# Kernel optimization log

Measured on AMD Instinct MI355X. Metric: run time of the kernel, lower is better.

The kernel has to match this reference:

```python
import jax, jax.numpy as jnp
import numpy as np

N_NODES = 100000
N_EDGES = 640000
HIDDEN = 128


def setup_inputs() -> dict:
    key = jax.random.key(0)
    k_h, k_e, k_w1, k_b1, k_w2, k_b2 = jax.random.split(key, 6)
    h = jax.random.normal(k_h, (N_NODES, HIDDEN), dtype=jnp.float32)
    edge_index = jax.random.randint(k_e, (2, N_EDGES), 0, N_NODES, dtype=jnp.int64)
    # nn.Linear default init: U(-1/sqrt(fan_in), 1/sqrt(fan_in))
    lim1 = 1.0 / np.sqrt(2 * HIDDEN)
    W1 = jax.random.uniform(k_w1, (2 * HIDDEN, HIDDEN), jnp.float32, -lim1, lim1)
    b1 = jax.random.uniform(k_b1, (HIDDEN,), jnp.float32, -lim1, lim1)
    lim2 = 1.0 / np.sqrt(HIDDEN)
    W2 = jax.random.uniform(k_w2, (HIDDEN, 1), jnp.float32, -lim2, lim2)
    b2 = jax.random.uniform(k_b2, (1,), jnp.float32, -lim2, lim2)
    return {"h": h, "edge_index": edge_index, "W1": W1, "b1": b1, "W2": W2, "b2": b2}


def reference(h, edge_index, W1, b1, W2, b2):
    src, dst = edge_index[0], edge_index[1]
    # cat([h[src], h[dst]]) @ W1 == h[src] @ W1[:H] + h[dst] @ W1[H:]
    W1s, W1d = W1[:HIDDEN], W1[HIDDEN:]
    x = h[src] @ W1s + h[dst] @ W1d + b1          # [E, H]
    x = jax.nn.relu(x)
    score = x @ W2 + b2                            # [E, 1]
    return score.squeeze(-1)                       # [E]
```

## Files before the change

### kernel.cpp

```cpp
#include <hip/hip_runtime.h>

#define HIDDEN 128

typedef _Float16 f16x8 __attribute__((ext_vector_type(8)));
typedef _Float16 f16x4 __attribute__((ext_vector_type(4)));
typedef _Float16 f16x2 __attribute__((ext_vector_type(2)));
typedef __fp16   fp16v2 __attribute__((ext_vector_type(2)));
typedef float f32x4 __attribute__((ext_vector_type(4)));

__global__ __launch_bounds__(64) void prep_w(const float* __restrict__ W1,
                                             _Float16* __restrict__ Wpk) {
  const int blk = blockIdx.x;
  const int jt = blk >> 2;
  const int kt = blk & 3;
  const int lane = threadIdx.x;
  const int col = jt * 16 + (lane & 15);
  const int kbase = kt * 32 + (lane >> 4) * 8;
  f16x8 v;
#pragma unroll
  for (int j = 0; j < 8; ++j) {
    const int k = kbase + j;
    const float w = (col < HIDDEN) ? W1[k * HIDDEN + col]
                                   : W1[(HIDDEN + k) * HIDDEN + (col - HIDDEN)];
    v[j] = (_Float16)w;
  }
  *reinterpret_cast<f16x8*>(Wpk + ((size_t)blk * 64 + lane) * 8) = v;
}

__global__ __launch_bounds__(256) void gemm_mfma_v9(
    const float* __restrict__ h, const _Float16* __restrict__ Wpk,
    const float* __restrict__ b1, _Float16* __restrict__ Af,
    _Float16* __restrict__ Bf, int n_nodes, int ntiles) {
  __shared__ __align__(16) char out_lds[4 * 16 * 528];

  const int tid = threadIdx.x;
  const int lane = tid & 63;
  const int wave = tid >> 6;
  const int nl = lane & 15;
  const int kgrp = lane >> 4;
  const int jt0 = wave * 4;
  const int t0 = blockIdx.x * 4;
  if (t0 >= ntiles) return;

  const f16x8* wp = reinterpret_cast<const f16x8*>(Wpk);
  f16x8 wfrag[4][4];
#pragma unroll
  for (int j4 = 0; j4 < 4; ++j4)
#pragma unroll
    for (int kt = 0; kt < 4; ++kt)
      wfrag[j4][kt] = wp[((jt0 + j4) * 4 + kt) * 64 + lane];

  f32x4 binit[4];
#pragma unroll
  for (int j4 = 0; j4 < 4; ++j4) {
    const int jt = jt0 + j4;
    if (jt < 8) {
      binit[j4] = *reinterpret_cast<const f32x4*>(b1 + jt * 16 + kgrp * 4);
    } else {
      binit[j4][0] = 0.f; binit[j4][1] = 0.f; binit[j4][2] = 0.f; binit[j4][3] = 0.f;
    }
  }

  float4 buf0[8], buf1[8];
  f16x8 hfrag[4];

  auto LOAD = [&](float4* buf, int tile) {
    int node = tile * 16 + nl;
    if (node >= n_nodes) node = 0;
    const float4* hp = reinterpret_cast<const float4*>(h) +
                       (size_t)node * 32 + kgrp * 2;
#pragma unroll
    for (int kt = 0; kt < 4; ++kt) {
      buf[kt * 2]     = hp[kt * 8];
      buf[kt * 2 + 1] = hp[kt * 8 + 1];
    }
  };

  auto CVT = [&](const float4* buf) {
#pragma unroll
    for (int kt = 0; kt < 4; ++kt) {
      const float4 v0 = buf[kt * 2];
      const float4 v1 = buf[kt * 2 + 1];
      const fp16v2 p0 = __builtin_amdgcn_cvt_pkrtz(v0.x, v0.y);
      const fp16v2 p1 = __builtin_amdgcn_cvt_pkrtz(v0.z, v0.w);
      const fp16v2 p2 = __builtin_amdgcn_cvt_pkrtz(v1.x, v1.y);
      const fp16v2 p3 = __builtin_amdgcn_cvt_pkrtz(v1.z, v1.w);
      hfrag[kt][0] = (_Float16)p0[0]; hfrag[kt][1] = (_Float16)p0[1];
      hfrag[kt][2] = (_Float16)p1[0]; hfrag[kt][3] = (_Float16)p1[1];
      hfrag[kt][4] = (_Float16)p2[0]; hfrag[kt][5] = (_Float16)p2[1];
      hfrag[kt][6] = (_Float16)p3[0]; hfrag[kt][7] = (_Float16)p3[1];
    }
  };

  auto COMPUTE_DSWRITE = [&](int i) {
    f32x4 acc[4];
#pragma unroll
    for (int j4 = 0; j4 < 4; ++j4) acc[j4] = binit[j4];
#pragma unroll
    for (int kt = 0; kt < 4; ++kt)
#pragma unroll
      for (int j4 = 0; j4 < 4; ++j4)
        acc[j4] = __builtin_amdgcn_mfma_f32_16x16x32_f16(
            wfrag[j4][kt], hfrag[kt], acc[j4], 0, 0, 0);
#pragma unroll
    for (int j4 = 0; j4 < 4; ++j4) {
      const int jt = jt0 + j4;
      const int byte = i * 8448 + nl * 528 +
                       ((jt & 7) * 16 + kgrp * 4) * 2 + ((jt >= 8) ? 256 : 0);
      f16x4 v;
      v[0] = (_Float16)acc[j4][0];
      v[1] = (_Float16)acc[j4][1];
      v[2] = (_Float16)acc[j4][2];
      v[3] = (_Float16)acc[j4][3];
      *reinterpret_cast<f16x4*>(out_lds + byte) = v;
    }
  };

  LOAD(buf0, t0);
  LOAD(buf1, t0 + 1);
  CVT(buf0); LOAD(buf0, t0 + 2); COMPUTE_DSWRITE(0);
  CVT(buf1); LOAD(buf1, t0 + 3); COMPUTE_DSWRITE(1);
  CVT(buf0);                     COMPUTE_DSWRITE(2);
  CVT(buf1);                     COMPUTE_DSWRITE(3);

  __syncthreads();

  const int cn = tid >> 4;
  const int seg = tid & 15;
#pragma unroll
  for (int i = 0; i < 4; ++i) {
    const int node = (t0 + i) * 16 + cn;
    if (node < n_nodes) {
      const f16x8 a = *reinterpret_cast<const f16x8*>(
          out_lds + i * 8448 + cn * 528 + seg * 16);
      const f16x8 b = *reinterpret_cast<const f16x8*>(
          out_lds + i * 8448 + cn * 528 + 256 + seg * 16);
      *reinterpret_cast<f16x8*>(Af + (size_t)node * HIDDEN + seg * 8) = a;
      *reinterpret_cast<f16x8*>(Bf + (size_t)node * HIDDEN + seg * 8) = b;
    }
  }
}

__global__ __launch_bounds__(256) void edge_score_v5(
    const int* __restrict__ ei, const _Float16* __restrict__ Af,
    const _Float16* __restrict__ Bf, const float* __restrict__ W2,
    const float* __restrict__ b2, float* __restrict__ out, int n_edges) {
  const int wid = (int)((blockIdx.x * 256 + threadIdx.x) >> 6);
  const int lane = threadIdx.x & 63;
  const int e0 = wid * 16;
  if (e0 >= n_edges) return;

  int srcs[16], dsts[16];
  if (e0 + 16 <= n_edges) {
    const int4* sp = reinterpret_cast<const int4*>(ei + e0);
    const int4* dp = reinterpret_cast<const int4*>(ei + n_edges + e0);
#pragma unroll
    for (int q = 0; q < 4; ++q) {
      const int4 s4 = sp[q], d4 = dp[q];
      srcs[q * 4] = s4.x; srcs[q * 4 + 1] = s4.y; srcs[q * 4 + 2] = s4.z; srcs[q * 4 + 3] = s4.w;
      dsts[q * 4] = d4.x; dsts[q * 4 + 1] = d4.y; dsts[q * 4 + 2] = d4.z; dsts[q * 4 + 3] = d4.w;
    }
  } else {
#pragma unroll
    for (int k = 0; k < 16; ++k) {
      const int e = (e0 + k < n_edges) ? e0 + k : n_edges - 1;
      srcs[k] = ei[e];
      dsts[k] = ei[n_edges + e];
    }
  }

  const char* Afc = (const char*)Af;
  const char* Bfc = (const char*)Bf;
  const unsigned int loff = (unsigned int)(lane << 2);

  f16x2 av[16], bv[16];
#pragma unroll
  for (int k = 0; k < 16; ++k) {
    av[k] = *reinterpret_cast<const f16x2*>(Afc + (((unsigned int)srcs[k] << 8) + loff));
    bv[k] = *reinterpret_cast<const f16x2*>(Bfc + (((unsigned int)dsts[k] << 8) + loff));
  }
  __builtin_amdgcn_sched_barrier(0);

  const float2 w2v = reinterpret_cast<const float2*>(W2)[lane];
  const fp16v2 w2h = __builtin_amdgcn_cvt_pkrtz(w2v.x, w2v.y);
  const _Float16 h0 = (_Float16)0.f;

  float p[16];
#pragma unroll
  for (int k = 0; k < 16; ++k) {
    f16x2 s = av[k] + bv[k];
    s[0] = s[0] > h0 ? s[0] : h0;
    s[1] = s[1] > h0 ? s[1] : h0;
    p[k] = __builtin_amdgcn_fdot2(__builtin_bit_cast(fp16v2, s), w2h, 0.f, false);
  }

  auto mrg = [&](float a, float b, int off) {
    const float as = a + __shfl_xor(a, off, 64);
    const float bs = b + __shfl_xor(b, off, 64);
    return (lane & off) ? bs : as;
  };
  float q[8];
#pragma unroll
  for (int i = 0; i < 8; ++i) q[i] = mrg(p[2 * i], p[2 * i + 1], 1);
  float r[4];
#pragma unroll
  for (int i = 0; i < 4; ++i) r[i] = mrg(q[2 * i], q[2 * i + 1], 2);
  float s2[2];
#pragma unroll
  for (int i = 0; i < 2; ++i) s2[i] = mrg(r[2 * i], r[2 * i + 1], 4);
  float t = mrg(s2[0], s2[1], 8);
  t += __shfl_xor(t, 16, 64);
  t += __shfl_xor(t, 32, 64);

  if (lane < 16 && e0 + lane < n_edges) out[e0 + lane] = t + b2[0];
}

__global__ __launch_bounds__(256) void fused_fallback(
    const float* __restrict__ h, const int* __restrict__ ei,
    const float* __restrict__ W1, const float* __restrict__ b1,
    const float* __restrict__ W2, const float* __restrict__ b2,
    float* __restrict__ out, int n_edges) {
  const int e = (int)((blockIdx.x * 256 + threadIdx.x) >> 6);
  const int lane = threadIdx.x & 63;
  if (e >= n_edges) return;
  const int src = ei[e], dst = ei[n_edges + e];
  const float* hs = h + (size_t)src * HIDDEN;
  const float* hd = h + (size_t)dst * HIDDEN;
  float acc0 = b1[lane], acc1 = b1[lane + 64];
  for (int k = 0; k < HIDDEN; ++k) {
    const float s = hs[k], d = hd[k];
    acc0 = fmaf(s, W1[k * HIDDEN + lane], acc0);
    acc0 = fmaf(d, W1[(k + HIDDEN) * HIDDEN + lane], acc0);
    acc1 = fmaf(s, W1[k * HIDDEN + lane + 64], acc1);
    acc1 = fmaf(d, W1[(k + HIDDEN) * HIDDEN + lane + 64], acc1);
  }
  acc0 = acc0 > 0.f ? acc0 : 0.f;
  acc1 = acc1 > 0.f ? acc1 : 0.f;
  float p = fmaf(acc0, W2[lane], acc1 * W2[lane + 64]);
#pragma unroll
  for (int off = 32; off >= 1; off >>= 1) p += __shfl_down(p, off, 64);
  if (lane == 0) out[e] = p + b2[0];
}

extern "C" void kernel_launch(void* const* d_in, const int* in_sizes, int n_in,
                              void* d_out, int out_size, void* d_ws, size_t ws_size,
                              hipStream_t stream) {
  const float* h  = (const float*)d_in[0];
  const int*   ei = (const int*)d_in[1];
  const float* W1 = (const float*)d_in[2];
  const float* b1 = (const float*)d_in[3];
  const float* W2 = (const float*)d_in[4];
  const float* b2 = (const float*)d_in[5];
  float* out = (float*)d_out;

  const int n_nodes = in_sizes[0] / HIDDEN;
  const int n_edges = in_sizes[1] / 2;

  const size_t wpk_halfs  = 64 * 64 * 8;
  const size_t proj_halfs = (size_t)n_nodes * HIDDEN;
  const size_t need = (wpk_halfs + 2 * proj_halfs) * sizeof(_Float16);

  if (ws_size >= need) {
    _Float16* Wpk = (_Float16*)d_ws;
    _Float16* A   = Wpk + wpk_halfs;
    _Float16* B   = A + proj_halfs;

    prep_w<<<64, 64, 0, stream>>>(W1, Wpk);

    const int ntiles = (n_nodes + 15) / 16;
    const int gblocks = (ntiles + 3) / 4;
    gemm_mfma_v9<<<gblocks, 256, 0, stream>>>(h, Wpk, b1, A, B, n_nodes, ntiles);

    const int nwaves = (n_edges + 15) / 16;
    const int eblocks = (nwaves + 3) / 4;
    edge_score_v5<<<eblocks, 256, 0, stream>>>(ei, A, B, W2, b2, out, n_edges);
  } else {
    const int eblocks = (n_edges + 3) / 4;
    fused_fallback<<<eblocks, 256, 0, stream>>>(h, ei, W1, b1, W2, b2, out, n_edges);
  }
}
```

Baseline: 89.16 us.

## Stage node rows through swizzled LDS with coalesced loads in projection GEMM

The node-projection kernel now has each block handle 32 nodes. Threads load h with fully coalesced float4 reads, convert to fp16 and store into an XOR-swizzled LDS staging buffer, and the MFMA operands are then read from that buffer. Before, each lane loaded strided fragments from global memory directly, with register double-buffering over 4 tiles. The new layout is meant to improve global load coalescing and raise block count/occupancy, at the cost of an extra barrier and the loss of load/compute overlap within a block. A scheduling barrier in the edge kernel is also removed.

```diff
diff --git a/kernel.cpp b/kernel.cpp
--- a/kernel.cpp
+++ b/kernel.cpp
@@ -27,11 +27,12 @@
   *reinterpret_cast<f16x8*>(Wpk + ((size_t)blk * 64 + lane) * 8) = v;
 }
 
-__global__ __launch_bounds__(256) void gemm_mfma_v9(
+__global__ __launch_bounds__(256) void gemm_mfma_v10(
     const float* __restrict__ h, const _Float16* __restrict__ Wpk,
     const float* __restrict__ b1, _Float16* __restrict__ Af,
-    _Float16* __restrict__ Bf, int n_nodes, int ntiles) {
-  __shared__ __align__(16) char out_lds[4 * 16 * 528];
+    _Float16* __restrict__ Bf, int n_nodes) {
+  __shared__ __align__(16) char stage[32 * 256];
+  __shared__ __align__(16) char obuf[32 * 528];
 
   const int tid = threadIdx.x;
   const int lane = tid & 63;
@@ -39,8 +40,7 @@
   const int nl = lane & 15;
   const int kgrp = lane >> 4;
   const int jt0 = wave * 4;
-  const int t0 = blockIdx.x * 4;
-  if (t0 >= ntiles) return;
+  const int node0 = blockIdx.x * 32;
 
   const f16x8* wp = reinterpret_cast<const f16x8*>(Wpk);
   f16x8 wfrag[4][4];
@@ -61,80 +61,77 @@
     }
   }
 
-  float4 buf0[8], buf1[8];
-  f16x8 hfrag[4];
-
-  auto LOAD = [&](float4* buf, int tile) {
-    int node = tile * 16 + nl;
-    if (node >= n_nodes) node = 0;
-    const float4* hp = reinterpret_cast<const float4*>(h) +
-                       (size_t)node * 32 + kgrp * 2;
+  float4 sbuf[4];
+#pragma unroll
+  for (int q = 0; q < 4; ++q) {
+    const int lin = q * 2048 + tid * 8;
+    int node = node0 + (lin >> 8);
+    if (node >= n_nodes) node = n_nodes - 1;
+    sbuf[q] = *reinterpret_cast<const float4*>(
+        reinterpret_cast<const char*>(h) + (size_t)node * 512 + (lin & 255) * 2);
+  }
+#pragma unroll
+  for (int q = 0; q < 4; ++q) {
+    const int lin = q * 2048 + tid * 8;
+    const int row = lin >> 8;
+    const int col = lin & 255;
+    const fp16v2 p0 = __builtin_amdgcn_cvt_pkrtz(sbuf[q].x, sbuf[q].y);
+    const fp16v2 p1 = __builtin_amdgcn_cvt_pkrtz(sbuf[q].z, sbuf[q].w);
+    f16x4 v;
+    v[0] = (_Float16)p0[0]; v[1] = (_Float16)p0[1];
+    v[2] = (_Float16)p1[0]; v[3] = (_Float16)p1[1];
+    const int dst = row * 256 + (col ^ ((row & 7) << 4));
+    *reinterpret_cast<f16x4*>(stage + dst) = v;
+  }
+  __syncthreads();
+
+  f32x4 acc[2][4];
+#pragma unroll
+  for (int s = 0; s < 2; ++s)
+#pragma unroll
+    for (int j4 = 0; j4 < 4; ++j4) acc[s][j4] = binit[j4];
+
+#pragma unroll
+  for (int s = 0; s < 2; ++s) {
+    const int row = s * 16 + nl;
 #pragma unroll
     for (int kt = 0; kt < 4; ++kt) {
-      buf[kt * 2]     = hp[kt * 8];
-      buf[kt * 2 + 1] = hp[kt * 8 + 1];
-    }
-  };
-
-  auto CVT = [&](const float4* buf) {
-#pragma unroll
-    for (int kt = 0; kt < 4; ++kt) {
-      const float4 v0 = buf[kt * 2];
-      const float4 v1 = buf[kt * 2 + 1];
-      const fp16v2 p0 = __builtin_amdgcn_cvt_pkrtz(v0.x, v0.y);
-      const fp16v2 p1 = __builtin_amdgcn_cvt_pkrtz(v0.z, v0.w);
-      const fp16v2 p2 = __builtin_amdgcn_cvt_pkrtz(v1.x, v1.y);
-      const fp16v2 p3 = __builtin_amdgcn_cvt_pkrtz(v1.z, v1.w);
-      hfrag[kt][0] = (_Float16)p0[0]; hfrag[kt][1] = (_Float16)p0[1];
-      hfrag[kt][2] = (_Float16)p1[0]; hfrag[kt][3] = (_Float16)p1[1];
-      hfrag[kt][4] = (_Float16)p2[0]; hfrag[kt][5] = (_Float16)p2[1];
-      hfrag[kt][6] = (_Float16)p3[0]; hfrag[kt][7] = (_Float16)p3[1];
-    }
-  };
-
-  auto COMPUTE_DSWRITE = [&](int i) {
-    f32x4 acc[4];
-#pragma unroll
-    for (int j4 = 0; j4 < 4; ++j4) acc[j4] = binit[j4];
-#pragma unroll
-    for (int kt = 0; kt < 4; ++kt)
+      const int addr = row * 256 + ((kt * 64 + kgrp * 16) ^ ((row & 7) << 4));
+      const f16x8 hf = *reinterpret_cast<const f16x8*>(stage + addr);
 #pragma unroll
       for (int j4 = 0; j4 < 4; ++j4)
-        acc[j4] = __builtin_amdgcn_mfma_f32_16x16x32_f16(
-            wfrag[j4][kt], hfrag[kt], acc[j4], 0, 0, 0);
+        acc[s][j4] = __builtin_amdgcn_mfma_f32_16x16x32_f16(
+            wfrag[j4][kt], hf, acc[s][j4], 0, 0, 0);
+    }
+  }
+
+#pragma unroll
+  for (int s = 0; s < 2; ++s) {
+    const int row = s * 16 + nl;
 #pragma unroll
     for (int j4 = 0; j4 < 4; ++j4) {
       const int jt = jt0 + j4;
-      const int byte = i * 8448 + nl * 528 +
-                       ((jt & 7) * 16 + kgrp * 4) * 2 + ((jt >= 8) ? 256 : 0);
+      const int byte = row * 528 + ((jt & 7) * 16 + kgrp * 4) * 2 +
+                       ((jt >= 8) ? 256 : 0);
       f16x4 v;
-      v[0] = (_Float16)acc[j4][0];
-      v[1] = (_Float16)acc[j4][1];
-      v[2] = (_Float16)acc[j4][2];
-      v[3] = (_Float16)acc[j4][3];
-      *reinterpret_cast<f16x4*>(out_lds + byte) = v;
-    }
-  };
-
-  LOAD(buf0, t0);
-  LOAD(buf1, t0 + 1);
-  CVT(buf0); LOAD(buf0, t0 + 2); COMPUTE_DSWRITE(0);
-  CVT(buf1); LOAD(buf1, t0 + 3); COMPUTE_DSWRITE(1);
-  CVT(buf0);                     COMPUTE_DSWRITE(2);
-  CVT(buf1);                     COMPUTE_DSWRITE(3);
-
+      v[0] = (_Float16)acc[s][j4][0];
+      v[1] = (_Float16)acc[s][j4][1];
+      v[2] = (_Float16)acc[s][j4][2];
+      v[3] = (_Float16)acc[s][j4][3];
+      *reinterpret_cast<f16x4*>(obuf + byte) = v;
+    }
+  }
   __syncthreads();
 
-  const int cn = tid >> 4;
+  const int cs = tid >> 4;
   const int seg = tid & 15;
 #pragma unroll
-  for (int i = 0; i < 4; ++i) {
-    const int node = (t0 + i) * 16 + cn;
+  for (int half = 0; half < 2; ++half) {
+    const int cn = half * 16 + cs;
+    const int node = node0 + cn;
     if (node < n_nodes) {
-      const f16x8 a = *reinterpret_cast<const f16x8*>(
-          out_lds + i * 8448 + cn * 528 + seg * 16);
-      const f16x8 b = *reinterpret_cast<const f16x8*>(
-          out_lds + i * 8448 + cn * 528 + 256 + seg * 16);
+      const f16x8 a = *reinterpret_cast<const f16x8*>(obuf + cn * 528 + seg * 16);
+      const f16x8 b = *reinterpret_cast<const f16x8*>(obuf + cn * 528 + 256 + seg * 16);
       *reinterpret_cast<f16x8*>(Af + (size_t)node * HIDDEN + seg * 8) = a;
       *reinterpret_cast<f16x8*>(Bf + (size_t)node * HIDDEN + seg * 8) = b;
     }
@@ -179,7 +176,6 @@
     av[k] = *reinterpret_cast<const f16x2*>(Afc + (((unsigned int)srcs[k] << 8) + loff));
     bv[k] = *reinterpret_cast<const f16x2*>(Bfc + (((unsigned int)dsts[k] << 8) + loff));
   }
-  __builtin_amdgcn_sched_barrier(0);
 
   const float2 w2v = reinterpret_cast<const float2*>(W2)[lane];
   const fp16v2 w2h = __builtin_amdgcn_cvt_pkrtz(w2v.x, w2v.y);
@@ -267,9 +263,8 @@
 
     prep_w<<<64, 64, 0, stream>>>(W1, Wpk);
 
-    const int ntiles = (n_nodes + 15) / 16;
-    const int gblocks = (ntiles + 3) / 4;
-    gemm_mfma_v9<<<gblocks, 256, 0, stream>>>(h, Wpk, b1, A, B, n_nodes, ntiles);
+    const int gblocks = (n_nodes + 31) / 32;
+    gemm_mfma_v10<<<gblocks, 256, 0, stream>>>(h, Wpk, b1, A, B, n_nodes);
 
     const int nwaves = (n_edges + 15) / 16;
     const int eblocks = (nwaves + 3) / 4;
```

Result: faster. 77.54 us (-13.0%).
